# Kernel optimization log

Measured on AMD Instinct MI355X. Metric: run time of the kernel, lower is better.

Reference implementation:

```python
import jax, jax.numpy as jnp
import numpy as np

INPUT_SHAPE = 640
NUM_CLASSES = 80
STRIDES = (8, 16, 32)
DIS = 2.5 * STRIDES[0]        # center-region half-size (pixels)
EPS = 1e-7
BIG = 1e5                      # penalty for non-(center&inbox) candidates
INF = 1e9                      # effectively excludes a pair from top-k / argmin
BS, MAX_GT, NGT_VALID = 32, 50, 20


def _bce(p, t):
    p = jnp.clip(p, EPS, 1.0 - EPS)
    return -t * jnp.log(p) - (1.0 - t) * jnp.log(1.0 - p)


def _decode(pred, stride):
    # pred [B, 5+nc, l, l] -> decoded [B, l*l, 5+nc] with boxes in pixels (cx,cy,w,h)
    B, C, l, _ = pred.shape
    p = jnp.transpose(pred, (0, 2, 3, 1))          # [B, l, l, C] (row=y, col=x)
    xy = jax.nn.sigmoid(p[..., :2])
    wh = p[..., 2:4]
    objcls = jax.nn.sigmoid(p[..., 4:])
    gx = jnp.arange(l, dtype=p.dtype)[None, :]      # ix varies along width
    gy = jnp.arange(l, dtype=p.dtype)[:, None]      # iy varies along height
    x = (gx + xy[..., 0]) * stride
    y = (gy + xy[..., 1]) * stride
    w = jnp.exp(wh[..., 0]) * stride
    h = jnp.exp(wh[..., 1]) * stride
    out = jnp.concatenate([jnp.stack([x, y, w, h], -1), objcls], -1)
    return out.reshape(B, l * l, C)


def _pairwise_iou(gt, pr):
    # gt [G,4], pr [A,4] in cxcywh -> [G,A]
    g_tl = gt[:, None, :2] - gt[:, None, 2:4] * 0.5
    g_br = gt[:, None, :2] + gt[:, None, 2:4] * 0.5
    p_tl = pr[None, :, :2] - pr[None, :, 2:4] * 0.5
    p_br = pr[None, :, :2] + pr[None, :, 2:4] * 0.5
    wh = jnp.maximum(jnp.minimum(g_br, p_br) - jnp.maximum(g_tl, p_tl), 0.0)
    inter = wh[..., 0] * wh[..., 1]
    union = gt[:, None, 2] * gt[:, None, 3] + pr[None, :, 2] * pr[None, :, 3] - inter
    return inter / jnp.clip(union, 1e-6)


def _region_mask(px, py, cx, cy, hw, hh):
    # anchor center inside (clipped) box around (cx,cy) with half-extents (hw,hh)
    left = jnp.maximum(cx - hw, 0.0)[:, None]
    right = jnp.minimum(cx + hw, float(INPUT_SHAPE))[:, None]
    top = jnp.maximum(cy - hh, 0.0)[:, None]
    bot = jnp.minimum(cy + hh, float(INPUT_SHAPE))[:, None]
    return (px[None] >= left) & (px[None] <= right) & (py[None] >= top) & (py[None] <= bot)


def _per_image(pred, tgt):
    # pred [A, 5+nc] decoded, tgt [G, 5+nc]
    G, A = tgt.shape[0], pred.shape[0]
    valid = tgt[:, 4] == 1.0
    px, py = pred[:, 0], pred[:, 1]
    cx, cy, gw, gh = tgt[:, 0], tgt[:, 1], tgt[:, 2], tgt[:, 3]

    center_m = _region_mask(px, py, cx, cy, DIS, DIS)
    inbox_m = _region_mask(px, py, cx, cy, gw * 0.5, gh * 0.5)
    or_m = (center_m | inbox_m) & valid[:, None]     # candidate anchors
    and_m = center_m & inbox_m & valid[:, None]      # preferred anchors

    iou = _pairwise_iou(tgt[:, :4], pred[:, :4])     # [G, A]
    iou_cost = -jnp.log(iou + 1e-8)

    # pairwise class BCE cost summed over classes, via matmul (one-hot targets)
    pcls = jnp.clip(pred[:, 5:], EPS, 1.0 - EPS)     # [A, nc]
    logp = jnp.log(pcls)
    log1mp = jnp.log(1.0 - pcls)
    tcls = tgt[:, 5:]                                 # [G, nc]
    cls_cost = tcls @ (log1mp - logp).T - log1mp.sum(-1)[None, :]  # [G, A]

    cost = cls_cost + 3.0 * iou_cost + BIG * (~and_m)
    cost_full = jnp.where(valid[:, None], cost, INF)
    cost_sel = jnp.where(or_m, cost, INF)

    # dynamic-k: sum of top-10 candidate IoUs, floored at 1, capped by #and-candidates
    k10 = jax.lax.top_k(iou * or_m.astype(iou.dtype), 10)[0].sum(-1)
    and_cnt = and_m.sum(-1)
    dk = jnp.minimum(jnp.maximum(k10.astype(jnp.int32), 1), jnp.maximum(and_cnt, 1))

    # take 10 lowest-cost anchors per GT, keep the first dk of them
    _, topi = jax.lax.top_k(-cost_sel, 10)            # [G, 10]
    keep = (jnp.arange(10)[None, :] < dk[:, None]) & valid[:, None]
    keep = keep & jnp.take_along_axis(or_m, topi, axis=1)
    assign = jnp.zeros((G, A), jnp.int32).at[jnp.arange(G)[:, None], topi].max(
        keep.astype(jnp.int32)) > 0                    # [G, A] bool

    overlap = assign.sum(0) > 1
    best = jnp.argmin(cost_full, axis=0)              # [A]
    onehot = jnp.arange(G)[:, None] == best[None, :]
    assign = jnp.where(overlap[None, :], onehot, assign)

    fg = assign.any(0)
    l_conf = _bce(pred[:, 4], fg.astype(pred.dtype)).sum()
    l_cls = jnp.sum(jnp.where(assign, cls_cost, 0.0))
    l_reg = jnp.sum(jnp.where(assign, 1.0 - iou ** 2, 0.0))
    return l_reg, l_conf, l_cls, valid.sum()


def setup_inputs() -> dict:
    key = jax.random.key(0)
    k1, k2, k3, k4, k5, k6, k7 = jax.random.split(key, 7)
    p8 = 0.5 * jax.random.normal(k1, (BS, 5 + NUM_CLASSES, 80, 80), jnp.float32)
    p16 = 0.5 * jax.random.normal(k2, (BS, 5 + NUM_CLASSES, 40, 40), jnp.float32)
    p32 = 0.5 * jax.random.normal(k3, (BS, 5 + NUM_CLASSES, 20, 20), jnp.float32)
    # targets: (cx, cy, w, h, valid_flag, one_hot_class)
    cxy = jax.random.uniform(k4, (BS, NGT_VALID, 2), jnp.float32, 32.0, INPUT_SHAPE - 32.0)
    wh = jax.random.uniform(k5, (BS, NGT_VALID, 2), jnp.float32, 16.0, 128.0)
    cls_idx = jax.random.randint(k6, (BS, NGT_VALID), 0, NUM_CLASSES)
    onehot = jax.nn.one_hot(cls_idx, NUM_CLASSES, dtype=jnp.float32)
    flag = jnp.ones((BS, NGT_VALID, 1), jnp.float32)
    valid_rows = jnp.concatenate([cxy, wh, flag, onehot], -1)   # [BS, 20, 85]
    pad = jnp.zeros((BS, MAX_GT - NGT_VALID, 5 + NUM_CLASSES), jnp.float32)
    targets = jnp.concatenate([valid_rows, pad], axis=1)        # [BS, 50, 85]
    return {"p8": p8, "p16": p16, "p32": p32, "targets": targets}


def reference(p8, p16, p32, targets):
    preds = jnp.concatenate(
        [_decode(p8, STRIDES[0]), _decode(p16, STRIDES[1]), _decode(p32, STRIDES[2])],
        axis=1)                                                  # [BS, 8400, 85]
    l_reg, l_conf, l_cls, ng = jax.vmap(_per_image)(preds, targets)
    num_gts = jnp.maximum(ng.sum(), 1).astype(preds.dtype)
    reg_weight = 5.0
    return (reg_weight * l_reg.sum() + l_cls.sum() + l_conf.sum()) / num_gts
```

## Files before the change

kernel.cpp:

```cpp
#include <hip/hip_runtime.h>
#include <math.h>

#define BSZ  32
#define GSZ  50
#define ATOT 8400
#define NCLS 80
#define CDIM 85
#define TPB  256
#define TPA  512
#define GRIDX ((ATOT + TPB - 1) / TPB)
#define NPART (GRIDX * BSZ)
#define MAXC 512

#define EPSF 1e-7f
#define BIGF 100000.0f
#define INFF 1000000000.0f
#define IMGF 640.0f
#define DISF 20.0f
#define LOGEPS_HI -15.942385f

__device__ __forceinline__ float fexp(float x){ return __expf(x); }
__device__ __forceinline__ float flog(float x){ return __logf(x); }

__device__ __forceinline__ float sigm(float z){ return 1.0f/(1.0f+fexp(-z)); }
__device__ __forceinline__ float clampp(float s){ return fminf(fmaxf(s, EPSF), 1.f-EPSF); }
__device__ __forceinline__ float log1msig(float z){
  return fmaxf(-flog(1.f + fexp(z)), LOGEPS_HI);
}

__device__ __forceinline__ const float* chan_ptr(const float* __restrict__ p8,
                                                 const float* __restrict__ p16,
                                                 const float* __restrict__ p32,
                                                 int b, int a, int ch){
  if (a < 6400) return p8  + ((size_t)(b*CDIM + ch))*6400 + a;
  if (a < 8000) return p16 + ((size_t)(b*CDIM + ch))*1600 + (a-6400);
  return p32 + ((size_t)(b*CDIM + ch))*400 + (a-8000);
}

__device__ __forceinline__ void compute_pair(
  float cx, float cy, float gw, float gh,
  float px, float py, float pw, float ph,
  float z, float slog,
  float& cost, float& iou, bool& orm, bool& andm, float& clsc)
{
  float hw = gw*0.5f, hh = gh*0.5f;
  bool cm = (px >= fmaxf(cx-DISF,0.f)) && (px <= fminf(cx+DISF,IMGF)) &&
            (py >= fmaxf(cy-DISF,0.f)) && (py <= fminf(cy+DISF,IMGF));
  bool im = (px >= fmaxf(cx-hw,0.f)) && (px <= fminf(cx+hw,IMGF)) &&
            (py >= fmaxf(cy-hh,0.f)) && (py <= fminf(cy+hh,IMGF));
  orm = cm || im;  andm = cm && im;
  float phw = pw*0.5f, phh = ph*0.5f;
  float wx = fmaxf(fminf(cx+hw, px+phw) - fmaxf(cx-hw, px-phw), 0.f);
  float wy = fmaxf(fminf(cy+hh, py+phh) - fmaxf(cy-hh, py-phh), 0.f);
  float inter = wx*wy;
  float uni   = gw*gh + pw*ph - inter;
  iou = inter / fmaxf(uni, 1e-6f);
  clsc = -z - slog;
  cost = clsc + 3.f*(-flog(iou + 1e-8f)) + (andm ? 0.f : BIGF);
}

__device__ __forceinline__ void acc_l1ms(float4& A, float4 w){
  A.x += log1msig(w.x); A.y += log1msig(w.y);
  A.z += log1msig(w.z); A.w += log1msig(w.w);
}

__global__ __launch_bounds__(TPB, 4)
void k_decode(const float* __restrict__ p8, const float* __restrict__ p16,
              const float* __restrict__ p32, const float* __restrict__ tgt,
              float* __restrict__ bx, float* __restrict__ by,
              float* __restrict__ bw, float* __restrict__ bh,
              float* __restrict__ obj, float* __restrict__ slog,
              unsigned long long* __restrict__ bits, int* __restrict__ cidx){
  int t = blockIdx.x*blockDim.x + threadIdx.x;
  int sub = t & 3;
  int g   = t >> 2;
  int b = g / (ATOT/4);
  int q = g % (ATOT/4);
  int a0 = q*4;
  const float* base; int l; float fs; int aL;
  if (a0 < 6400){ base = p8;  l = 80; fs = 8.f;  aL = a0; }
  else if (a0 < 8000){ base = p16; l = 40; fs = 16.f; aL = a0-6400; }
  else { base = p32; l = 20; fs = 32.f; aL = a0-8000; }
  int l2 = l*l;
  int cs = l2 >> 2;
  const float4* p4 = (const float4*)(base + (size_t)b*CDIM*l2) + (aL >> 2);

  const float4* cp = p4 + (size_t)(5+sub)*cs;
  const size_t st4 = (size_t)4*cs;
  float4 A0 = make_float4(0.f,0.f,0.f,0.f);
  float4 A1 = A0, A2 = A0, A3 = A0;
  #pragma unroll
  for (int k = 0; k < 20; k += 4){
    float4 w0 = cp[(size_t)(k+0)*st4];
    float4 w1 = cp[(size_t)(k+1)*st4];
    float4 w2 = cp[(size_t)(k+2)*st4];
    float4 w3 = cp[(size_t)(k+3)*st4];
    acc_l1ms(A0, w0); acc_l1ms(A1, w1); acc_l1ms(A2, w2); acc_l1ms(A3, w3);
  }
  float4 S = make_float4(A0.x+A1.x+A2.x+A3.x, A0.y+A1.y+A2.y+A3.y,
                         A0.z+A1.z+A2.z+A3.z, A0.w+A1.w+A2.w+A3.w);
  #pragma unroll
  for (int m = 1; m <= 2; m <<= 1){
    S.x += __shfl_xor(S.x, m, 64);
    S.y += __shfl_xor(S.y, m, 64);
    S.z += __shfl_xor(S.z, m, 64);
    S.w += __shfl_xor(S.w, m, 64);
  }

  int i = aL / l, j = aL % l;
  float fi = (float)i;
  uint4 z4 = make_uint4(0u,0u,0u,0u);
  if (sub == 0){
    float4 v0 = p4[0];
    float4 v4 = p4[4*cs];
    ((float4*)bx)[g]  = make_float4(((float)(j  )+sigm(v0.x))*fs, ((float)(j+1)+sigm(v0.y))*fs,
                                    ((float)(j+2)+sigm(v0.z))*fs, ((float)(j+3)+sigm(v0.w))*fs);
    ((float4*)obj)[g] = make_float4(sigm(v4.x), sigm(v4.y), sigm(v4.z), sigm(v4.w));
    ((uint4*)bits)[2*g] = z4;
  } else if (sub == 1){
    float4 v1 = p4[cs];
    ((float4*)by)[g]   = make_float4((fi+sigm(v1.x))*fs, (fi+sigm(v1.y))*fs,
                                     (fi+sigm(v1.z))*fs, (fi+sigm(v1.w))*fs);
    ((float4*)slog)[g] = S;
  } else if (sub == 2){
    float4 v2 = p4[2*cs];
    ((float4*)bw)[g] = make_float4(fexp(v2.x)*fs, fexp(v2.y)*fs, fexp(v2.z)*fs, fexp(v2.w)*fs);
    ((uint4*)bits)[2*g+1] = z4;
  } else {
    float4 v3 = p4[3*cs];
    ((float4*)bh)[g] = make_float4(fexp(v3.x)*fs, fexp(v3.y)*fs, fexp(v3.z)*fs, fexp(v3.w)*fs);
  }

  if (t < BSZ*GSZ){
    const float* Tq = tgt + (size_t)t*CDIM;
    int best = 0; float bv = Tq[5];
    for (int c = 1; c < NCLS; c++){
      float vv = Tq[5+c];
      if (vv > bv){ bv = vv; best = c; }
    }
    cidx[t] = best;
  }
}

__device__ __forceinline__ unsigned f2u(float f){
  unsigned u = __float_as_uint(f);
  return (u & 0x80000000u) ? ~u : (u | 0x80000000u);
}

__global__ __launch_bounds__(TPA)
void k_assign(const float* __restrict__ p8, const float* __restrict__ p16,
              const float* __restrict__ p32, const float* __restrict__ tgt,
              const int* __restrict__ cidx,
              const float* __restrict__ bx, const float* __restrict__ by,
              const float* __restrict__ bw, const float* __restrict__ bh,
              const float* __restrict__ slog,
              unsigned long long* __restrict__ bits){
  int g = blockIdx.x, b = blockIdx.y;
  const float* T = tgt + ((size_t)b*GSZ + g)*CDIM;
  if (T[4] != 1.0f) return;
  float cx = T[0], cy = T[1], gw = T[2], gh = T[3];
  float hw = gw*0.5f, hh = gh*0.5f;
  float cL = fmaxf(cx-DISF,0.f), cR = fminf(cx+DISF,IMGF);
  float cT = fmaxf(cy-DISF,0.f), cB = fminf(cy+DISF,IMGF);
  float iL = fmaxf(cx-hw,0.f),  iR = fminf(cx+hw,IMGF);
  float iT = fmaxf(cy-hh,0.f),  iB = fminf(cy+hh,IMGF);
  float gArea = gw*gh;
  int ch = 5 + cidx[b*GSZ + g];
  int t = threadIdx.x;
  int lane = t & 63, wave = t >> 6;

  const float* BX = bx + (size_t)b*ATOT;
  const float* BY = by + (size_t)b*ATOT;
  const float* BW = bw + (size_t)b*ATOT;
  const float* BH = bh + (size_t)b*ATOT;
  const float* SL = slog + (size_t)b*ATOT;

  float ux = fmaxf(DISF, hw), uy = fmaxf(DISF, hh);
  float RL = fmaxf(cx-ux, 0.f), RR = fminf(cx+ux, IMGF);
  float RT = fmaxf(cy-uy, 0.f), RB = fminf(cy+uy, IMGF);

  auto rect = [&](float inv, int l, int& j0r, int& i0r, int& wr, int& hr){
    int a_ = (int)floorf(RL*inv) - 1; if (a_ < 0) a_ = 0;
    int b_ = (int)floorf(RR*inv) + 1; if (b_ > l-1) b_ = l-1;
    int c_ = (int)floorf(RT*inv) - 1; if (c_ < 0) c_ = 0;
    int d_ = (int)floorf(RB*inv) + 1; if (d_ > l-1) d_ = l-1;
    j0r = a_; i0r = c_; wr = b_-a_+1; hr = d_-c_+1;
  };
  int j0_0,i0_0,w_0,h_0, j0_1,i0_1,w_1,h_1, j0_2,i0_2,w_2,h_2;
  rect(0.125f,   80, j0_0,i0_0,w_0,h_0);
  rect(0.0625f,  40, j0_1,i0_1,w_1,h_1);
  rect(0.03125f, 20, j0_2,i0_2,w_2,h_2);
  int o1 = w_0*h_0, o2 = o1 + w_1*h_1, ntot = o2 + w_2*h_2;

  __shared__ int cand[MAXC];
  __shared__ int ncand_sh;
  __shared__ int wand[TPA/64];
  if (t == 0) ncand_sh = 0;
  __syncthreads();

  int myand = 0;
  for (int cell = t; cell < ntot; cell += TPA){
    int v = (cell >= o1) + (cell >= o2);
    int loc, jj0, ii0, ww, ll, ab;
    if (v == 0){ loc = cell;    jj0=j0_0; ii0=i0_0; ww=w_0; ll=80; ab=0;    }
    else if (v == 1){ loc = cell-o1; jj0=j0_1; ii0=i0_1; ww=w_1; ll=40; ab=6400; }
    else { loc = cell-o2; jj0=j0_2; ii0=i0_2; ww=w_2; ll=20; ab=8000; }
    int ii = ii0 + loc / ww;
    int jj = jj0 + loc % ww;
    int a  = ab + ii*ll + jj;
    float px = BX[a], py = BY[a];
    bool cm = (px >= cL) && (px <= cR) && (py >= cT) && (py <= cB);
    bool im = (px >= iL) && (px <= iR) && (py >= iT) && (py <= iB);
    bool orm = cm || im, andm = cm && im;
    unsigned long long mo = __ballot(orm);
    myand += __popcll(__ballot(andm));
    if (orm){
      int leader = __ffsll((long long)mo) - 1;
      int base = 0;
      if (lane == leader) base = atomicAdd(&ncand_sh, __popcll(mo));
      base = __shfl(base, leader, 64);
      int pos = base + __popcll(mo & ((1ull << lane) - 1ull));
      if (pos < MAXC) cand[pos] = a | (andm ? 0x10000 : 0);
    }
  }
  if (lane == 0) wand[wave] = myand;
  __syncthreads();
  int nc = ncand_sh < MAXC ? ncand_sh : MAXC;

  unsigned long long ck; float io;
  if (t < nc){
    int packed = cand[t];
    int a = packed & 0xFFFF;
    bool andm = (packed & 0x10000) != 0;
    float px = BX[a], py = BY[a];
    float pw = BW[a], ph = BH[a];
    float phw = pw*0.5f, phh = ph*0.5f;
    float wx = fmaxf(fminf(cx+hw, px+phw) - fmaxf(cx-hw, px-phw), 0.f);
    float wy = fmaxf(fminf(cy+hh, py+phh) - fmaxf(cy-hh, py-phh), 0.f);
    float inter = wx*wy;
    io = inter / fmaxf(gArea + pw*ph - inter, 1e-6f);
    float z = *chan_ptr(p8, p16, p32, b, a, ch);
    float cost = (-z - SL[a]) + 3.f*(-flog(io + 1e-8f)) + (andm ? 0.f : BIGF);
    ck = ((unsigned long long)f2u(cost) << 32) | (unsigned)a;
  } else {
    ck = ~0ull; io = -1.f;
  }

  __shared__ unsigned long long skey[(TPA/64)*10];
  __shared__ float siou[(TPA/64)*10];
  bool wactive = (wave << 6) < nc;
  if (wactive){
    #pragma unroll
    for (int k = 2; k <= 64; k <<= 1){
      #pragma unroll
      for (int j = k >> 1; j > 0; j >>= 1){
        unsigned long long ok = __shfl_xor(ck, j, 64);
        float oi = __shfl_xor(io, j, 64);
        bool tmin = (((lane & k) == 0) == ((lane & j) == 0));
        ck = tmin ? (ck < ok ? ck : ok) : (ck > ok ? ck : ok);
        io = tmin ? fmaxf(io, oi) : fminf(io, oi);
      }
    }
  }
  if (lane < 10){
    skey[wave*10 + lane] = wactive ? ck : ~0ull;
    siou[wave*10 + lane] = wactive ? io : -1.f;
  }
  __syncthreads();

  if (t == 0){
    int and_cnt = 0;
    #pragma unroll
    for (int q = 0; q < TPA/64; q++) and_cnt += wand[q];
    float k10 = 0.f;
    {
      int h[TPA/64] = {0,0,0,0,0,0,0,0};
      for (int r = 0; r < 10; r++){
        float v = -2.f; int w = -1;
        #pragma unroll
        for (int q = 0; q < TPA/64; q++){
          if (h[q] < 10){
            float vq = siou[q*10 + h[q]];
            if (vq > v){ v = vq; w = q; }
          }
        }
        if (w >= 0) h[w]++;
        k10 += fmaxf(v, 0.f);
      }
    }
    int dk = (int)k10;
    if (dk < 1) dk = 1;
    int ub = and_cnt > 1 ? and_cnt : 1;
    if (dk > ub) dk = ub;
    int h[TPA/64] = {0,0,0,0,0,0,0,0};
    for (int r = 0; r < dk && r < 10; r++){
      unsigned long long bestk = ~0ull; int w = -1;
      #pragma unroll
      for (int q = 0; q < TPA/64; q++){
        if (h[q] < 10){
          unsigned long long kq = skey[q*10 + h[q]];
          if (kq < bestk){ bestk = kq; w = q; }
        }
      }
      if (bestk == ~0ull) break;
      h[w]++;
      int idx = (int)(bestk & 0xFFFFFFFFull);
      atomicOr(&bits[(size_t)b*ATOT + idx], 1ull << g);
    }
  }
}

__global__ void k_loss(const float* __restrict__ p8, const float* __restrict__ p16,
                       const float* __restrict__ p32, const float* __restrict__ tgt,
                       const int* __restrict__ cidx,
                       const float* __restrict__ bx, const float* __restrict__ by,
                       const float* __restrict__ bw, const float* __restrict__ bh,
                       const float* __restrict__ obj, const float* __restrict__ slog,
                       const unsigned long long* __restrict__ bits,
                       float* __restrict__ partials){
  int b = blockIdx.y;
  int a = blockIdx.x*TPB + threadIdx.x;
  __shared__ float gcx[GSZ], gcy[GSZ], ggw[GSZ], ggh[GSZ], gval[GSZ];
  __shared__ int gci[GSZ];
  for (int k = threadIdx.x; k < GSZ; k += TPB){
    const float* T = tgt + ((size_t)b*GSZ + k)*CDIM;
    gcx[k] = T[0]; gcy[k] = T[1]; ggw[k] = T[2]; ggh[k] = T[3]; gval[k] = T[4];
    gci[k] = cidx[b*GSZ + k];
  }
  __syncthreads();

  float contrib = 0.f;
  if (a < ATOT){
    size_t t = (size_t)b*ATOT + a;
    unsigned long long m = bits[t];
    float o = clampp(obj[t]);
    if (m == 0ull){
      contrib = -flog(1.f - o);
    } else {
      float px = bx[t], py = by[t], pw = bw[t], ph = bh[t], sl = slog[t];
      if (__builtin_popcountll(m) > 1){
        float bestc = INFF; int bestg = 0;
        for (int g = 0; g < GSZ; g++){
          float c = INFF;
          if (gval[g] == 1.0f){
            float z = *chan_ptr(p8, p16, p32, b, a, 5+gci[g]);
            float iou, clsc; bool orm, andm;
            compute_pair(gcx[g], gcy[g], ggw[g], ggh[g], px, py, pw, ph, z, sl,
                         c, iou, orm, andm, clsc);
          }
          if (c < bestc){ bestc = c; bestg = g; }
        }
        m = 1ull << bestg;
      }
      contrib = -flog(o);
      while (m){
        int g = __builtin_ctzll(m);
        m &= m - 1;
        float z = *chan_ptr(p8, p16, p32, b, a, 5+gci[g]);
        float c, iou, clsc; bool orm, andm;
        compute_pair(gcx[g], gcy[g], ggw[g], ggh[g], px, py, pw, ph, z, sl,
                     c, iou, orm, andm, clsc);
        contrib += clsc + 5.f*(1.f - iou*iou);
      }
    }
  }

  #pragma unroll
  for (int s2 = 32; s2 > 0; s2 >>= 1) contrib += __shfl_xor(contrib, s2, 64);
  __shared__ float wsum[4];
  if ((threadIdx.x & 63) == 0) wsum[threadIdx.x >> 6] = contrib;
  __syncthreads();
  if (threadIdx.x == 0)
    partials[blockIdx.y*GRIDX + blockIdx.x] = wsum[0]+wsum[1]+wsum[2]+wsum[3];
}

__global__ void k_final(const float* __restrict__ partials,
                        const float* __restrict__ tgt, float* __restrict__ out){
  int t = threadIdx.x;
  float s = 0.f;
  for (int i = t; i < NPART; i += TPB) s += partials[i];
  int n = 0;
  for (int i = t; i < BSZ*GSZ; i += TPB)
    n += (tgt[(size_t)i*CDIM + 4] == 1.0f) ? 1 : 0;
  __shared__ float sh[TPB]; __shared__ int shn[TPB];
  sh[t] = s; shn[t] = n;
  __syncthreads();
  for (int st = TPB/2; st > 0; st >>= 1){
    if (t < st){ sh[t] += sh[t+st]; shn[t] += shn[t+st]; }
    __syncthreads();
  }
  if (t == 0){
    int nn = shn[0] < 1 ? 1 : shn[0];
    out[0] = sh[0] / (float)nn;
  }
}

extern "C" void kernel_launch(void* const* d_in, const int* in_sizes, int n_in,
                              void* d_out, int out_size, void* d_ws, size_t ws_size,
                              hipStream_t stream) {
  const float* p8  = (const float*)d_in[0];
  const float* p16 = (const float*)d_in[1];
  const float* p32 = (const float*)d_in[2];
  const float* tgt = (const float*)d_in[3];
  float* out = (float*)d_out;

  const size_t BA = (size_t)BSZ*ATOT;
  float* bx   = (float*)d_ws;
  float* by   = bx + BA;
  float* bw   = by + BA;
  float* bh   = bw + BA;
  float* obj  = bh + BA;
  float* slog = obj + BA;
  unsigned long long* bits = (unsigned long long*)(slog + BA);
  int* cidx = (int*)(bits + BA);
  float* partials = (float*)(cidx + BSZ*GSZ);

  dim3 blk(TPB);
  k_decode<<<dim3((unsigned)(BA/TPB)), blk, 0, stream>>>(p8, p16, p32, tgt,
                                                   bx, by, bw, bh, obj, slog, bits, cidx);
  k_assign<<<dim3(GSZ, BSZ), dim3(TPA), 0, stream>>>(p8, p16, p32, tgt, cidx,
                                               bx, by, bw, bh, slog, bits);
  k_loss  <<<dim3(GRIDX, BSZ), blk, 0, stream>>>(p8, p16, p32, tgt, cidx,
                                               bx, by, bw, bh, obj, slog, bits, partials);
  k_final <<<1, blk, 0, stream>>>(partials, tgt, out);
}
```

Measured before the change: 152.4 us.

## Fuse final reduction into loss kernel, prefetch decode loads, use log2 accumulation

Removes the separate final-reduction kernel: the last block of the loss kernel, found through an atomic counter, sums the partials and the precomputed valid-gt flags. The decode kernel now issues its box and objectness loads up front, software-pipelines the class-logit loads, and accumulates log-sigmoid terms in base 2 with a single ln2 rescale at the end. It also replaces the runtime division for grid coordinates with per-level constant divisors. These trade one kernel launch and some ALU work for an atomic and fence per block and slightly different rounding in the clamp.

```diff
diff --git a/kernel.cpp b/kernel.cpp
--- a/kernel.cpp
+++ b/kernel.cpp
@@ -18,14 +18,20 @@
 #define IMGF 640.0f
 #define DISF 20.0f
 #define LOGEPS_HI -15.942385f
+#define LN2F 0.69314718056f
 
 __device__ __forceinline__ float fexp(float x){ return __expf(x); }
 __device__ __forceinline__ float flog(float x){ return __logf(x); }
 
 __device__ __forceinline__ float sigm(float z){ return 1.0f/(1.0f+fexp(-z)); }
 __device__ __forceinline__ float clampp(float s){ return fminf(fmaxf(s, EPSF), 1.f-EPSF); }
-__device__ __forceinline__ float log1msig(float z){
-  return fmaxf(-flog(1.f + fexp(z)), LOGEPS_HI);
+
+__device__ __forceinline__ float l1ms2(float z){
+  return fmaxf(-__log2f(1.f + fexp(z)), -23.0f);
+}
+__device__ __forceinline__ void acc2(float4& A, float4 w){
+  A.x += l1ms2(w.x); A.y += l1ms2(w.y);
+  A.z += l1ms2(w.z); A.w += l1ms2(w.w);
 }
 
 __device__ __forceinline__ const float* chan_ptr(const float* __restrict__ p8,
@@ -59,43 +65,47 @@
   cost = clsc + 3.f*(-flog(iou + 1e-8f)) + (andm ? 0.f : BIGF);
 }
 
-__device__ __forceinline__ void acc_l1ms(float4& A, float4 w){
-  A.x += log1msig(w.x); A.y += log1msig(w.y);
-  A.z += log1msig(w.z); A.w += log1msig(w.w);
-}
-
 __global__ __launch_bounds__(TPB, 4)
 void k_decode(const float* __restrict__ p8, const float* __restrict__ p16,
               const float* __restrict__ p32, const float* __restrict__ tgt,
               float* __restrict__ bx, float* __restrict__ by,
               float* __restrict__ bw, float* __restrict__ bh,
               float* __restrict__ obj, float* __restrict__ slog,
-              unsigned long long* __restrict__ bits, int* __restrict__ cidx){
+              unsigned long long* __restrict__ bits, int* __restrict__ cidx,
+              int* __restrict__ vflag, unsigned* __restrict__ done){
   int t = blockIdx.x*blockDim.x + threadIdx.x;
   int sub = t & 3;
   int g   = t >> 2;
   int b = g / (ATOT/4);
   int q = g % (ATOT/4);
   int a0 = q*4;
-  const float* base; int l; float fs; int aL;
-  if (a0 < 6400){ base = p8;  l = 80; fs = 8.f;  aL = a0; }
-  else if (a0 < 8000){ base = p16; l = 40; fs = 16.f; aL = a0-6400; }
-  else { base = p32; l = 20; fs = 32.f; aL = a0-8000; }
+  const float* base; int l; float fs; int aL; int ii, jj;
+  if (a0 < 6400){ base = p8;  l = 80; fs = 8.f;  aL = a0;      ii = aL/80; jj = aL - ii*80; }
+  else if (a0 < 8000){ base = p16; l = 40; fs = 16.f; aL = a0-6400; ii = aL/40; jj = aL - ii*40; }
+  else { base = p32; l = 20; fs = 32.f; aL = a0-8000; ii = aL/20; jj = aL - ii*20; }
   int l2 = l*l;
   int cs = l2 >> 2;
   const float4* p4 = (const float4*)(base + (size_t)b*CDIM*l2) + (aL >> 2);
+
+  float4 vA = p4[(size_t)sub*cs];
+  float4 vB = p4[(size_t)4*cs];
 
   const float4* cp = p4 + (size_t)(5+sub)*cs;
   const size_t st4 = (size_t)4*cs;
   float4 A0 = make_float4(0.f,0.f,0.f,0.f);
   float4 A1 = A0, A2 = A0, A3 = A0;
+  float4 w0 = cp[0], w1 = cp[st4], w2 = cp[2*st4], w3 = cp[3*st4];
   #pragma unroll
   for (int k = 0; k < 20; k += 4){
-    float4 w0 = cp[(size_t)(k+0)*st4];
-    float4 w1 = cp[(size_t)(k+1)*st4];
-    float4 w2 = cp[(size_t)(k+2)*st4];
-    float4 w3 = cp[(size_t)(k+3)*st4];
-    acc_l1ms(A0, w0); acc_l1ms(A1, w1); acc_l1ms(A2, w2); acc_l1ms(A3, w3);
+    float4 n0, n1, n2, n3;
+    if (k + 4 < 20){
+      n0 = cp[(size_t)(k+4)*st4];
+      n1 = cp[(size_t)(k+5)*st4];
+      n2 = cp[(size_t)(k+6)*st4];
+      n3 = cp[(size_t)(k+7)*st4];
+    }
+    acc2(A0, w0); acc2(A1, w1); acc2(A2, w2); acc2(A3, w3);
+    if (k + 4 < 20){ w0 = n0; w1 = n1; w2 = n2; w3 = n3; }
   }
   float4 S = make_float4(A0.x+A1.x+A2.x+A3.x, A0.y+A1.y+A2.y+A3.y,
                          A0.z+A1.z+A2.z+A3.z, A0.w+A1.w+A2.w+A3.w);
@@ -107,28 +117,22 @@
     S.w += __shfl_xor(S.w, m, 64);
   }
 
-  int i = aL / l, j = aL % l;
-  float fi = (float)i;
+  float fi = (float)ii;
   uint4 z4 = make_uint4(0u,0u,0u,0u);
   if (sub == 0){
-    float4 v0 = p4[0];
-    float4 v4 = p4[4*cs];
-    ((float4*)bx)[g]  = make_float4(((float)(j  )+sigm(v0.x))*fs, ((float)(j+1)+sigm(v0.y))*fs,
-                                    ((float)(j+2)+sigm(v0.z))*fs, ((float)(j+3)+sigm(v0.w))*fs);
-    ((float4*)obj)[g] = make_float4(sigm(v4.x), sigm(v4.y), sigm(v4.z), sigm(v4.w));
+    ((float4*)bx)[g]  = make_float4(((float)(jj  )+sigm(vA.x))*fs, ((float)(jj+1)+sigm(vA.y))*fs,
+                                    ((float)(jj+2)+sigm(vA.z))*fs, ((float)(jj+3)+sigm(vA.w))*fs);
+    ((float4*)obj)[g] = make_float4(sigm(vB.x), sigm(vB.y), sigm(vB.z), sigm(vB.w));
     ((uint4*)bits)[2*g] = z4;
   } else if (sub == 1){
-    float4 v1 = p4[cs];
-    ((float4*)by)[g]   = make_float4((fi+sigm(v1.x))*fs, (fi+sigm(v1.y))*fs,
-                                     (fi+sigm(v1.z))*fs, (fi+sigm(v1.w))*fs);
-    ((float4*)slog)[g] = S;
+    ((float4*)by)[g]   = make_float4((fi+sigm(vA.x))*fs, (fi+sigm(vA.y))*fs,
+                                     (fi+sigm(vA.z))*fs, (fi+sigm(vA.w))*fs);
+    ((float4*)slog)[g] = make_float4(S.x*LN2F, S.y*LN2F, S.z*LN2F, S.w*LN2F);
   } else if (sub == 2){
-    float4 v2 = p4[2*cs];
-    ((float4*)bw)[g] = make_float4(fexp(v2.x)*fs, fexp(v2.y)*fs, fexp(v2.z)*fs, fexp(v2.w)*fs);
+    ((float4*)bw)[g] = make_float4(fexp(vA.x)*fs, fexp(vA.y)*fs, fexp(vA.z)*fs, fexp(vA.w)*fs);
     ((uint4*)bits)[2*g+1] = z4;
   } else {
-    float4 v3 = p4[3*cs];
-    ((float4*)bh)[g] = make_float4(fexp(v3.x)*fs, fexp(v3.y)*fs, fexp(v3.z)*fs, fexp(v3.w)*fs);
+    ((float4*)bh)[g] = make_float4(fexp(vA.x)*fs, fexp(vA.y)*fs, fexp(vA.z)*fs, fexp(vA.w)*fs);
   }
 
   if (t < BSZ*GSZ){
@@ -139,7 +143,9 @@
       if (vv > bv){ bv = vv; best = c; }
     }
     cidx[t] = best;
-  }
+    vflag[t] = (Tq[4] == 1.0f) ? 1 : 0;
+  }
+  if (t == 0) *done = 0u;
 }
 
 __device__ __forceinline__ unsigned f2u(float f){
@@ -317,7 +323,8 @@
                        const float* __restrict__ bw, const float* __restrict__ bh,
                        const float* __restrict__ obj, const float* __restrict__ slog,
                        const unsigned long long* __restrict__ bits,
-                       float* __restrict__ partials){
+                       float* __restrict__ partials, const int* __restrict__ vflag,
+                       unsigned* __restrict__ done, float* __restrict__ out){
   int b = blockIdx.y;
   int a = blockIdx.x*TPB + threadIdx.x;
   __shared__ float gcx[GSZ], gcy[GSZ], ggw[GSZ], ggh[GSZ], gval[GSZ];
@@ -372,26 +379,34 @@
   __syncthreads();
   if (threadIdx.x == 0)
     partials[blockIdx.y*GRIDX + blockIdx.x] = wsum[0]+wsum[1]+wsum[2]+wsum[3];
-}
-
-__global__ void k_final(const float* __restrict__ partials,
-                        const float* __restrict__ tgt, float* __restrict__ out){
-  int t = threadIdx.x;
-  float s = 0.f;
-  for (int i = t; i < NPART; i += TPB) s += partials[i];
-  int n = 0;
-  for (int i = t; i < BSZ*GSZ; i += TPB)
-    n += (tgt[(size_t)i*CDIM + 4] == 1.0f) ? 1 : 0;
-  __shared__ float sh[TPB]; __shared__ int shn[TPB];
-  sh[t] = s; shn[t] = n;
-  __syncthreads();
-  for (int st = TPB/2; st > 0; st >>= 1){
-    if (t < st){ sh[t] += sh[t+st]; shn[t] += shn[t+st]; }
+
+  __shared__ unsigned lastf;
+  __threadfence();
+  if (threadIdx.x == 0){
+    unsigned old = atomicAdd(done, 1u);
+    lastf = (old == (unsigned)(NPART-1)) ? 1u : 0u;
+  }
+  __syncthreads();
+  if (lastf){
+    __threadfence();
+    float s = 0.f;
+    for (int i = threadIdx.x; i < NPART; i += TPB) s += partials[i];
+    int n = 0;
+    for (int i = threadIdx.x; i < BSZ*GSZ; i += TPB) n += vflag[i];
+    #pragma unroll
+    for (int s2 = 32; s2 > 0; s2 >>= 1){
+      s += __shfl_xor(s, s2, 64);
+      n += __shfl_xor(n, s2, 64);
+    }
+    __shared__ float fsm[4]; __shared__ int fnm[4];
+    if ((threadIdx.x & 63) == 0){ fsm[threadIdx.x >> 6] = s; fnm[threadIdx.x >> 6] = n; }
     __syncthreads();
-  }
-  if (t == 0){
-    int nn = shn[0] < 1 ? 1 : shn[0];
-    out[0] = sh[0] / (float)nn;
+    if (threadIdx.x == 0){
+      float tot = fsm[0]+fsm[1]+fsm[2]+fsm[3];
+      int nn = fnm[0]+fnm[1]+fnm[2]+fnm[3];
+      if (nn < 1) nn = 1;
+      out[0] = tot / (float)nn;
+    }
   }
 }
 
@@ -414,13 +429,16 @@
   unsigned long long* bits = (unsigned long long*)(slog + BA);
   int* cidx = (int*)(bits + BA);
   float* partials = (float*)(cidx + BSZ*GSZ);
+  int* vflag = (int*)(partials + NPART);
+  unsigned* done = (unsigned*)(vflag + BSZ*GSZ);
 
   dim3 blk(TPB);
   k_decode<<<dim3((unsigned)(BA/TPB)), blk, 0, stream>>>(p8, p16, p32, tgt,
-                                                   bx, by, bw, bh, obj, slog, bits, cidx);
+                                                   bx, by, bw, bh, obj, slog, bits,
+                                                   cidx, vflag, done);
   k_assign<<<dim3(GSZ, BSZ), dim3(TPA), 0, stream>>>(p8, p16, p32, tgt, cidx,
                                                bx, by, bw, bh, slog, bits);
   k_loss  <<<dim3(GRIDX, BSZ), blk, 0, stream>>>(p8, p16, p32, tgt, cidx,
-                                               bx, by, bw, bh, obj, slog, bits, partials);
-  k_final <<<1, blk, 0, stream>>>(partials, tgt, out);
-}
+                                               bx, by, bw, bh, obj, slog, bits,
+                                               partials, vflag, done, out);
+}
```

New measurement: 216.8 us. +42.3%, slower.
